# Kernel optimization log

Hardware: AMD Instinct MI355X
Metric: run time of the kernel (lower is better)

Reference implementation:

```python
import jax, jax.numpy as jnp
import numpy as np

N_NODES = 100000
N_EDGES = 1600000
IN_FEAT = 128
N_HEADS = 8
OUT_FEAT = 16


def setup_inputs() -> dict:
    key = jax.random.key(0)
    k1, k2, k3, k4, k5 = jax.random.split(key, 5)
    x = jax.random.normal(k1, (N_NODES, IN_FEAT), dtype=jnp.float32)
    edge_index = jax.random.randint(k2, (2, N_EDGES), 0, N_NODES)
    # Glorot-uniform params as in init_params
    lim_w = float(np.sqrt(6.0 / (IN_FEAT + N_HEADS * OUT_FEAT)))
    W = jax.random.uniform(k3, (IN_FEAT, N_HEADS * OUT_FEAT), minval=-lim_w, maxval=lim_w, dtype=jnp.float32)
    lim_a = float(np.sqrt(6.0 / (1 + N_HEADS * OUT_FEAT)))
    a_src = jax.random.uniform(k4, (N_HEADS, OUT_FEAT), minval=-lim_a, maxval=lim_a, dtype=jnp.float32)
    a_tgt = jax.random.uniform(k5, (N_HEADS, OUT_FEAT), minval=-lim_a, maxval=lim_a, dtype=jnp.float32)
    bias = jnp.zeros((OUT_FEAT,), dtype=jnp.float32)
    return {"in_nodes_features": x, "edge_index": edge_index, "W": W, "a_src": a_src, "a_tgt": a_tgt, "bias": bias}


def reference(in_nodes_features, edge_index, W, a_src, a_tgt, bias):
    # Single GATLayerImp3 with concat=False, activation=Softmax (GAT, num_of_layers=2).
    # Dropout disabled (eval / dropout=0.0).
    N = in_nodes_features.shape[0]
    H, F = a_src.shape
    proj = (in_nodes_features @ W).reshape(N, H, F)            # [N, H, F]
    s_src = jnp.einsum('nhf,hf->nh', proj, a_src)              # [N, H]
    s_tgt = jnp.einsum('nhf,hf->nh', proj, a_tgt)              # [N, H]
    src, tgt = edge_index[0], edge_index[1]
    # lift + per-edge LeakyReLU(0.2) scoring
    e = jax.nn.leaky_relu(s_src[src] + s_tgt[tgt], negative_slope=0.2)  # [E, H]
    # numerically stable segment softmax over edges sharing a target node
    seg_max = jax.ops.segment_max(e, tgt, num_segments=N)      # [N, H]
    seg_max = jnp.where(jnp.isfinite(seg_max), seg_max, 0.0)
    ex = jnp.exp(e - seg_max[tgt])                             # [E, H]
    denom = jax.ops.segment_sum(ex, tgt, num_segments=N)       # [N, H]
    alpha = ex / (denom[tgt] + 1e-16)                          # [E, H]
    # weighted message + scatter-add aggregation
    msg = proj[src] * alpha[:, :, None]                        # [E, H, F]
    out = jax.ops.segment_sum(msg, tgt, num_segments=N)        # [N, H, F]
    out = out.mean(axis=1) + bias                              # concat=False -> mean over heads
    return jax.nn.softmax(out, axis=-1)                        # final-layer Softmax activation
```

## Files before the change

### kernel.cpp

```cpp
#include <hip/hip_runtime.h>

#define NN 100000
#define NE 1600000

static __device__ __forceinline__ unsigned short f32_to_bf16_rne(float x) {
    unsigned int u = __float_as_uint(x);
    u += 0x7fff + ((u >> 16) & 1);
    return (unsigned short)(u >> 16);
}
static __device__ __forceinline__ float bf16_to_f32(unsigned int bits16) {
    return __uint_as_float(bits16 << 16);
}

__global__ __launch_bounds__(256) void gemm_score_kernel(const float* __restrict__ x,
                                                         const float* __restrict__ W,
                                                         const float* __restrict__ a_src,
                                                         const float* __restrict__ a_tgt,
                                                         unsigned short* __restrict__ projT,
                                                         float* __restrict__ s_src,
                                                         float* __restrict__ pack) {
    __shared__ float sXT[32][68];
    __shared__ float sW[32][128];
    const int t = threadIdx.x;
    const int n0 = blockIdx.x * 64;
    const int c0 = (t & 31) * 4;
    const int r0 = t >> 5;
    float acc[8][4];
#pragma unroll
    for (int i = 0; i < 8; i++)
#pragma unroll
        for (int j = 0; j < 4; j++) acc[i][j] = 0.f;

    for (int kt = 0; kt < 128; kt += 32) {
#pragma unroll
        for (int p = 0; p < 2; p++) {
            int idx = t + p * 256;
            int r = idx >> 3;
            int kk = idx & 7;
            float4 v = make_float4(0.f, 0.f, 0.f, 0.f);
            int n = n0 + r;
            if (n < NN) v = *reinterpret_cast<const float4*>(&x[(size_t)n * 128 + kt + kk * 4]);
            sXT[kk * 4 + 0][r] = v.x;
            sXT[kk * 4 + 1][r] = v.y;
            sXT[kk * 4 + 2][r] = v.z;
            sXT[kk * 4 + 3][r] = v.w;
        }
#pragma unroll
        for (int p = 0; p < 4; p++) {
            int idx = t + p * 256;
            int kr = idx >> 5;
            int c4 = idx & 31;
            float4 v = *reinterpret_cast<const float4*>(&W[(size_t)(kt + kr) * 128 + c4 * 4]);
            *reinterpret_cast<float4*>(&sW[kr][c4 * 4]) = v;
        }
        __syncthreads();
#pragma unroll
        for (int k = 0; k < 32; k++) {
            float4 xa = *reinterpret_cast<const float4*>(&sXT[k][r0 * 8]);
            float4 xb = *reinterpret_cast<const float4*>(&sXT[k][r0 * 8 + 4]);
            float4 wv = *reinterpret_cast<const float4*>(&sW[k][c0]);
            float xs[8] = {xa.x, xa.y, xa.z, xa.w, xb.x, xb.y, xb.z, xb.w};
#pragma unroll
            for (int i = 0; i < 8; i++) {
                acc[i][0] += xs[i] * wv.x;
                acc[i][1] += xs[i] * wv.y;
                acc[i][2] += xs[i] * wv.z;
                acc[i][3] += xs[i] * wv.w;
            }
        }
        __syncthreads();
    }
    const int h  = c0 >> 4;
    const int f0 = c0 & 15;
    const float aS0 = a_src[c0], aS1 = a_src[c0 + 1], aS2 = a_src[c0 + 2], aS3 = a_src[c0 + 3];
    const float aT0 = a_tgt[c0], aT1 = a_tgt[c0 + 1], aT2 = a_tgt[c0 + 2], aT3 = a_tgt[c0 + 3];
#pragma unroll
    for (int i = 0; i < 8; i++) {
        int n = n0 + r0 * 8 + i;
        if (n < NN) {
            unsigned short* pT = &projT[(size_t)n * 128];
#pragma unroll
            for (int j = 0; j < 4; j++) pT[(f0 + j) * 8 + h] = f32_to_bf16_rne(acc[i][j]);
            float ss = acc[i][0] * aS0 + acc[i][1] * aS1 + acc[i][2] * aS2 + acc[i][3] * aS3;
            float st = acc[i][0] * aT0 + acc[i][1] * aT1 + acc[i][2] * aT2 + acc[i][3] * aT3;
            ss += __shfl_xor(ss, 1);
            ss += __shfl_xor(ss, 2);
            st += __shfl_xor(st, 1);
            st += __shfl_xor(st, 2);
            if ((t & 3) == 0) {
                s_src[(size_t)n * 8 + h] = ss;
                pack[(size_t)n * 16 + h] = st;
            }
        }
    }
}

__global__ __launch_bounds__(256) void denom_kernel(const int* __restrict__ src,
                                                    const int* __restrict__ tgt,
                                                    const float* __restrict__ s_src,
                                                    float* __restrict__ pack) {
    int gid = blockIdx.x * blockDim.x + threadIdx.x;
    int e = gid >> 3;
    if (e >= NE) return;
    int h = gid & 7;
    int s = src[e], t = tgt[e];
    float v = s_src[(size_t)s * 8 + h] + pack[(size_t)t * 16 + h];
    v = v >= 0.f ? v : 0.2f * v;
    atomicAdd(&pack[(size_t)t * 16 + 8 + h], expf(v));
}

__global__ __launch_bounds__(256) void aggregate_kernel(const int* __restrict__ src,
                                                        const int* __restrict__ tgt,
                                                        const float* __restrict__ s_src,
                                                        const float* __restrict__ pack,
                                                        const unsigned short* __restrict__ projT,
                                                        float* __restrict__ out_acc) {
    int gid = blockIdx.x * blockDim.x + threadIdx.x;
    int e = gid >> 4;
    int lane = gid & 15;
    if (e >= NE) return;
    int s = src[e], t = tgt[e];
    int h = lane & 7;
    float eh = s_src[(size_t)s * 8 + h] + pack[(size_t)t * 16 + h];
    eh = eh >= 0.f ? eh : 0.2f * eh;
    float ex = expf(eh);
    float alpha = ex / (pack[(size_t)t * 16 + 8 + h] + 1e-16f);
    uint4 v = *reinterpret_cast<const uint4*>(&projT[(size_t)s * 128 + lane * 8]);
    float p0 = bf16_to_f32(v.x & 0xffffu), p1 = bf16_to_f32(v.x >> 16);
    float p2 = bf16_to_f32(v.y & 0xffffu), p3 = bf16_to_f32(v.y >> 16);
    float p4 = bf16_to_f32(v.z & 0xffffu), p5 = bf16_to_f32(v.z >> 16);
    float p6 = bf16_to_f32(v.w & 0xffffu), p7 = bf16_to_f32(v.w >> 16);
    float m = 0.f;
    m += __shfl(alpha, 0, 16) * p0;
    m += __shfl(alpha, 1, 16) * p1;
    m += __shfl(alpha, 2, 16) * p2;
    m += __shfl(alpha, 3, 16) * p3;
    m += __shfl(alpha, 4, 16) * p4;
    m += __shfl(alpha, 5, 16) * p5;
    m += __shfl(alpha, 6, 16) * p6;
    m += __shfl(alpha, 7, 16) * p7;
    atomicAdd(&out_acc[(size_t)t * 16 + lane], m * 0.125f);
}

__global__ __launch_bounds__(256) void softmax_kernel(const float* __restrict__ out_acc,
                                                      const float* __restrict__ bias,
                                                      float* __restrict__ out) {
    int gid = blockIdx.x * blockDim.x + threadIdx.x;
    int n = gid >> 4;
    int lane = gid & 15;
    if (n >= NN) return;
    float v = out_acc[(size_t)n * 16 + lane] + bias[lane];
    float mx = v;
#pragma unroll
    for (int m = 1; m < 16; m <<= 1) mx = fmaxf(mx, __shfl_xor(mx, m, 64));
    float ex = expf(v - mx);
    float sum = ex;
#pragma unroll
    for (int m = 1; m < 16; m <<= 1) sum += __shfl_xor(sum, m, 64);
    out[(size_t)n * 16 + lane] = ex / sum;
}

extern "C" void kernel_launch(void* const* d_in, const int* in_sizes, int n_in,
                              void* d_out, int out_size, void* d_ws, size_t ws_size,
                              hipStream_t stream) {
    const float* x     = (const float*)d_in[0];
    const int*   ei    = (const int*)d_in[1];
    const float* W     = (const float*)d_in[2];
    const float* a_src = (const float*)d_in[3];
    const float* a_tgt = (const float*)d_in[4];
    const float* bias  = (const float*)d_in[5];
    float* out = (float*)d_out;

    const int* src = ei;
    const int* tgt = ei + NE;

    char* ws = (char*)d_ws;
    size_t off = 0;
    auto alloc = [&](size_t bytes) {
        char* p = ws + off;
        off += (bytes + 255) & ~(size_t)255;
        return p;
    };
    unsigned short* projT   = (unsigned short*)alloc((size_t)NN * 128 * 2);
    float*          s_src   = (float*)alloc((size_t)NN * 8 * 4);
    float*          pack    = (float*)alloc((size_t)NN * 16 * 4);
    float*          out_acc = (float*)alloc((size_t)NN * 16 * 4);

    hipMemsetAsync(pack, 0, (size_t)NN * 16 * 4, stream);
    hipMemsetAsync(out_acc, 0, (size_t)NN * 16 * 4, stream);

    gemm_score_kernel<<<(NN + 63) / 64, 256, 0, stream>>>(x, W, a_src, a_tgt, projT, s_src, pack);
    denom_kernel<<<((size_t)NE * 8 + 255) / 256, 256, 0, stream>>>(src, tgt, s_src, pack);
    aggregate_kernel<<<((size_t)NE * 16 + 255) / 256, 256, 0, stream>>>(src, tgt, s_src, pack,
                                                                        projT, out_acc);
    softmax_kernel<<<(NN * 16 + 255) / 256, 256, 0, stream>>>(out_acc, bias, out);
}
```

Before: 269.9 us.

## Build CSR by target on device and fuse denominator, aggregation, softmax per node

Replaces the edge-parallel atomic denominator and aggregation kernels with a per-call CSR build (degree histogram, three-kernel scan, atomic scatter of source ids). A single node-parallel kernel then computes the softmax denominator, the weighted sum and the final softmax without float atomics. This removes the 25.6M float atomics and the out_acc round trip. In exchange it adds several small launches and integer atomics, and the per-node loops are unbalanced across varying degrees. The scatter order is nondeterministic, so the order of floating-point summation varies between runs.

Result: slower. 365.5 us (+35.4%).

```diff
diff --git a/kernel.cpp b/kernel.cpp
--- a/kernel.cpp
+++ b/kernel.cpp
@@ -18,7 +18,7 @@
                                                          const float* __restrict__ a_tgt,
                                                          unsigned short* __restrict__ projT,
                                                          float* __restrict__ s_src,
-                                                         float* __restrict__ pack) {
+                                                         float* __restrict__ s_tgt) {
     __shared__ float sXT[32][68];
     __shared__ float sW[32][128];
     const int t = threadIdx.x;
@@ -89,75 +89,145 @@
             st += __shfl_xor(st, 2);
             if ((t & 3) == 0) {
                 s_src[(size_t)n * 8 + h] = ss;
-                pack[(size_t)n * 16 + h] = st;
+                s_tgt[(size_t)n * 8 + h] = st;
             }
         }
     }
 }
 
-__global__ __launch_bounds__(256) void denom_kernel(const int* __restrict__ src,
-                                                    const int* __restrict__ tgt,
-                                                    const float* __restrict__ s_src,
-                                                    float* __restrict__ pack) {
+__global__ __launch_bounds__(256) void hist_kernel(const int* __restrict__ tgt,
+                                                   int* __restrict__ deg) {
+    int e = blockIdx.x * blockDim.x + threadIdx.x;
+    if (e >= NE) return;
+    atomicAdd(&deg[tgt[e]], 1);
+}
+
+__global__ __launch_bounds__(256) void scan_partial_kernel(const int* __restrict__ deg,
+                                                           int* __restrict__ tmp,
+                                                           int* __restrict__ blocksum) {
+    __shared__ int sdata[256];
+    const int b = blockIdx.x, t = threadIdx.x;
+    const int base = b * 1024 + t * 4;
+    int d[4], s = 0;
+#pragma unroll
+    for (int j = 0; j < 4; j++) {
+        int i = base + j;
+        d[j] = (i < NN) ? deg[i] : 0;
+        s += d[j];
+    }
+    sdata[t] = s;
+    __syncthreads();
+    for (int off = 1; off < 256; off <<= 1) {
+        int v = (t >= off) ? sdata[t - off] : 0;
+        __syncthreads();
+        sdata[t] += v;
+        __syncthreads();
+    }
+    int excl = sdata[t] - s;
+    int run = excl;
+#pragma unroll
+    for (int j = 0; j < 4; j++) {
+        int i = base + j;
+        if (i < NN) tmp[i] = run;
+        run += d[j];
+    }
+    if (t == 255) blocksum[b] = sdata[255];
+}
+
+#define NBLK_SCAN 98
+__global__ __launch_bounds__(128) void scan_blocksums_kernel(int* __restrict__ blocksum) {
+    __shared__ int sdata[128];
+    const int t = threadIdx.x;
+    int v = (t < NBLK_SCAN) ? blocksum[t] : 0;
+    sdata[t] = v;
+    __syncthreads();
+    for (int off = 1; off < 128; off <<= 1) {
+        int u = (t >= off) ? sdata[t - off] : 0;
+        __syncthreads();
+        sdata[t] += u;
+        __syncthreads();
+    }
+    if (t < NBLK_SCAN) blocksum[t] = sdata[t] - v;
+}
+
+__global__ __launch_bounds__(256) void scan_finalize_kernel(const int* __restrict__ tmp,
+                                                            const int* __restrict__ blocksum,
+                                                            int* __restrict__ row_start,
+                                                            int* __restrict__ cursor) {
+    int i = blockIdx.x * blockDim.x + threadIdx.x;
+    if (i >= NN) return;
+    int rs = tmp[i] + blocksum[i >> 10];
+    row_start[i] = rs;
+    cursor[i] = rs;
+}
+
+__global__ __launch_bounds__(256) void scatter_kernel(const int* __restrict__ src,
+                                                      const int* __restrict__ tgt,
+                                                      int* __restrict__ cursor,
+                                                      int* __restrict__ csr_src) {
+    int e = blockIdx.x * blockDim.x + threadIdx.x;
+    if (e >= NE) return;
+    int pos = atomicAdd(&cursor[tgt[e]], 1);
+    csr_src[pos] = src[e];
+}
+
+__global__ __launch_bounds__(256) void fused_agg_kernel(const int* __restrict__ row_start,
+                                                        const int* __restrict__ deg,
+                                                        const int* __restrict__ csr_src,
+                                                        const float* __restrict__ s_src,
+                                                        const float* __restrict__ s_tgt,
+                                                        const unsigned short* __restrict__ projT,
+                                                        const float* __restrict__ bias,
+                                                        float* __restrict__ out) {
     int gid = blockIdx.x * blockDim.x + threadIdx.x;
-    int e = gid >> 3;
-    if (e >= NE) return;
-    int h = gid & 7;
-    int s = src[e], t = tgt[e];
-    float v = s_src[(size_t)s * 8 + h] + pack[(size_t)t * 16 + h];
-    v = v >= 0.f ? v : 0.2f * v;
-    atomicAdd(&pack[(size_t)t * 16 + 8 + h], expf(v));
-}
-
-__global__ __launch_bounds__(256) void aggregate_kernel(const int* __restrict__ src,
-                                                        const int* __restrict__ tgt,
-                                                        const float* __restrict__ s_src,
-                                                        const float* __restrict__ pack,
-                                                        const unsigned short* __restrict__ projT,
-                                                        float* __restrict__ out_acc) {
-    int gid = blockIdx.x * blockDim.x + threadIdx.x;
-    int e = gid >> 4;
+    int t = gid >> 4;
     int lane = gid & 15;
-    if (e >= NE) return;
-    int s = src[e], t = tgt[e];
-    int h = lane & 7;
-    float eh = s_src[(size_t)s * 8 + h] + pack[(size_t)t * 16 + h];
-    eh = eh >= 0.f ? eh : 0.2f * eh;
-    float ex = expf(eh);
-    float alpha = ex / (pack[(size_t)t * 16 + 8 + h] + 1e-16f);
-    uint4 v = *reinterpret_cast<const uint4*>(&projT[(size_t)s * 128 + lane * 8]);
-    float p0 = bf16_to_f32(v.x & 0xffffu), p1 = bf16_to_f32(v.x >> 16);
-    float p2 = bf16_to_f32(v.y & 0xffffu), p3 = bf16_to_f32(v.y >> 16);
-    float p4 = bf16_to_f32(v.z & 0xffffu), p5 = bf16_to_f32(v.z >> 16);
-    float p6 = bf16_to_f32(v.w & 0xffffu), p7 = bf16_to_f32(v.w >> 16);
+    if (t >= NN) return;
+    const int h = lane & 7;
+    const int start = row_start[t];
+    const int dg = deg[t];
+    const float st = s_tgt[(size_t)t * 8 + h];
+
+    float dh = 0.f;
+    for (int i = (lane >> 3); i < dg; i += 2) {
+        int s = csr_src[start + i];
+        float v = s_src[(size_t)s * 8 + h] + st;
+        v = v >= 0.f ? v : 0.2f * v;
+        dh += expf(v);
+    }
+    dh += __shfl_xor(dh, 8, 16);
+    const float inv_d = 1.f / (dh + 1e-16f);
+
     float m = 0.f;
-    m += __shfl(alpha, 0, 16) * p0;
-    m += __shfl(alpha, 1, 16) * p1;
-    m += __shfl(alpha, 2, 16) * p2;
-    m += __shfl(alpha, 3, 16) * p3;
-    m += __shfl(alpha, 4, 16) * p4;
-    m += __shfl(alpha, 5, 16) * p5;
-    m += __shfl(alpha, 6, 16) * p6;
-    m += __shfl(alpha, 7, 16) * p7;
-    atomicAdd(&out_acc[(size_t)t * 16 + lane], m * 0.125f);
-}
-
-__global__ __launch_bounds__(256) void softmax_kernel(const float* __restrict__ out_acc,
-                                                      const float* __restrict__ bias,
-                                                      float* __restrict__ out) {
-    int gid = blockIdx.x * blockDim.x + threadIdx.x;
-    int n = gid >> 4;
-    int lane = gid & 15;
-    if (n >= NN) return;
-    float v = out_acc[(size_t)n * 16 + lane] + bias[lane];
+    for (int i = 0; i < dg; i++) {
+        int s = csr_src[start + i];
+        float eh = s_src[(size_t)s * 8 + h] + st;
+        eh = eh >= 0.f ? eh : 0.2f * eh;
+        float alpha = expf(eh) * inv_d;
+        uint4 v = *reinterpret_cast<const uint4*>(&projT[(size_t)s * 128 + lane * 8]);
+        float p0 = bf16_to_f32(v.x & 0xffffu), p1 = bf16_to_f32(v.x >> 16);
+        float p2 = bf16_to_f32(v.y & 0xffffu), p3 = bf16_to_f32(v.y >> 16);
+        float p4 = bf16_to_f32(v.z & 0xffffu), p5 = bf16_to_f32(v.z >> 16);
+        float p6 = bf16_to_f32(v.w & 0xffffu), p7 = bf16_to_f32(v.w >> 16);
+        m += __shfl(alpha, 0, 16) * p0;
+        m += __shfl(alpha, 1, 16) * p1;
+        m += __shfl(alpha, 2, 16) * p2;
+        m += __shfl(alpha, 3, 16) * p3;
+        m += __shfl(alpha, 4, 16) * p4;
+        m += __shfl(alpha, 5, 16) * p5;
+        m += __shfl(alpha, 6, 16) * p6;
+        m += __shfl(alpha, 7, 16) * p7;
+    }
+
+    float v = m * 0.125f + bias[lane];
     float mx = v;
 #pragma unroll
-    for (int m = 1; m < 16; m <<= 1) mx = fmaxf(mx, __shfl_xor(mx, m, 64));
+    for (int mm = 1; mm < 16; mm <<= 1) mx = fmaxf(mx, __shfl_xor(mx, mm, 16));
     float ex = expf(v - mx);
     float sum = ex;
 #pragma unroll
-    for (int m = 1; m < 16; m <<= 1) sum += __shfl_xor(sum, m, 64);
-    out[(size_t)n * 16 + lane] = ex / sum;
+    for (int mm = 1; mm < 16; mm <<= 1) sum += __shfl_xor(sum, mm, 16);
+    out[(size_t)t * 16 + lane] = ex / sum;
 }
 
 extern "C" void kernel_launch(void* const* d_in, const int* in_sizes, int n_in,
@@ -181,17 +251,24 @@
         off += (bytes + 255) & ~(size_t)255;
         return p;
     };
-    unsigned short* projT   = (unsigned short*)alloc((size_t)NN * 128 * 2);
-    float*          s_src   = (float*)alloc((size_t)NN * 8 * 4);
-    float*          pack    = (float*)alloc((size_t)NN * 16 * 4);
-    float*          out_acc = (float*)alloc((size_t)NN * 16 * 4);
-
-    hipMemsetAsync(pack, 0, (size_t)NN * 16 * 4, stream);
-    hipMemsetAsync(out_acc, 0, (size_t)NN * 16 * 4, stream);
-
-    gemm_score_kernel<<<(NN + 63) / 64, 256, 0, stream>>>(x, W, a_src, a_tgt, projT, s_src, pack);
-    denom_kernel<<<((size_t)NE * 8 + 255) / 256, 256, 0, stream>>>(src, tgt, s_src, pack);
-    aggregate_kernel<<<((size_t)NE * 16 + 255) / 256, 256, 0, stream>>>(src, tgt, s_src, pack,
-                                                                        projT, out_acc);
-    softmax_kernel<<<(NN * 16 + 255) / 256, 256, 0, stream>>>(out_acc, bias, out);
-}
+    unsigned short* projT     = (unsigned short*)alloc((size_t)NN * 128 * 2);
+    float*          s_src     = (float*)alloc((size_t)NN * 8 * 4);
+    float*          s_tgt     = (float*)alloc((size_t)NN * 8 * 4);
+    int*            deg       = (int*)alloc((size_t)NN * 4);
+    int*            tmp       = (int*)alloc((size_t)NN * 4);
+    int*            blocksum  = (int*)alloc((size_t)NBLK_SCAN * 4);
+    int*            row_start = (int*)alloc((size_t)NN * 4);
+    int*            cursor    = (int*)alloc((size_t)NN * 4);
+    int*            csr_src   = (int*)alloc((size_t)NE * 4);
+
+    hipMemsetAsync(deg, 0, (size_t)NN * 4, stream);
+
+    gemm_score_kernel<<<(NN + 63) / 64, 256, 0, stream>>>(x, W, a_src, a_tgt, projT, s_src, s_tgt);
+    hist_kernel<<<(NE + 255) / 256, 256, 0, stream>>>(tgt, deg);
+    scan_partial_kernel<<<NBLK_SCAN, 256, 0, stream>>>(deg, tmp, blocksum);
+    scan_blocksums_kernel<<<1, 128, 0, stream>>>(blocksum);
+    scan_finalize_kernel<<<(NN + 255) / 256, 256, 0, stream>>>(tmp, blocksum, row_start, cursor);
+    scatter_kernel<<<(NE + 255) / 256, 256, 0, stream>>>(src, tgt, cursor, csr_src);
+    fused_agg_kernel<<<((size_t)NN * 16 + 255) / 256, 256, 0, stream>>>(row_start, deg, csr_src,
+                                                                        s_src, s_tgt, projT, bias, out);
+}
```
